# Kernel tuning notes

Measured on AMD Instinct MI355X. Metric: run time of the kernel, lower is better.

Reference implementation:

```python
import jax, jax.numpy as jnp
import numpy as np

NUM_HEADS = 4
LN_EPS = 1e-5


def rotate_half(x):
    x1 = x[..., ::2]
    x2 = x[..., 1::2]
    return jnp.stack((-x2, x1), axis=-1).reshape(x.shape)


def apply_rope(freqs, t):
    # freqs: [2, B, 1, S, hd] (cos, sin); t: [B, H, S, hd]
    return t * freqs[0] + rotate_half(t) * freqs[1]


def normalize_kpts(kpts):
    size = 1.0 + kpts.max(-2) - kpts.min(-2)          # [B, 2]
    shift = size / 2.0
    scale = size.max(-1) / 2.0                         # [B]
    return (kpts - shift[..., None, :]) / scale[..., None, None]


def posenc(kpts, Wr):
    proj = kpts @ Wr                                   # [B, S, hd//2]
    emb = jnp.stack([jnp.cos(proj), jnp.sin(proj)], 0)[:, :, None, :, :]  # [2,B,1,S,hd//2]
    return jnp.repeat(emb, 2, axis=-1)                 # [2, B, 1, S, hd]


def layer_norm(x, g, b):
    mu = x.mean(-1, keepdims=True)
    var = ((x - mu) ** 2).mean(-1, keepdims=True)
    return (x - mu) / jnp.sqrt(var + LN_EPS) * g + b


def ffn(x, W1, b1, g, bt, W2, b2):
    return jax.nn.gelu(layer_norm(x @ W1 + b1, g, bt), approximate=False) @ W2 + b2


def heads_split(t, H):  # [B,S,D] -> [B,H,S,hd]
    B, S, D = t.shape
    return t.reshape(B, S, H, D // H).transpose(0, 2, 1, 3)


def heads_merge(t):  # [B,H,S,hd] -> [B,S,D]
    B, H, S, hd = t.shape
    return t.transpose(0, 2, 1, 3).reshape(B, S, H * hd)


def self_block(x, enc, Wqkv, bqkv, Wo, bo, W1, b1, g, bt, W2, b2):
    B, S, D = x.shape
    H = NUM_HEADS
    hd = D // H
    qkv = (x @ Wqkv + bqkv).reshape(B, S, H, hd, 3).transpose(0, 2, 1, 3, 4)
    q, k, v = qkv[..., 0], qkv[..., 1], qkv[..., 2]
    q = apply_rope(enc, q)
    k = apply_rope(enc, k)
    sim = jnp.einsum('bhid,bhjd->bhij', q, k) * (hd ** -0.5)
    ctx = jnp.einsum('bhij,bhjd->bhid', jax.nn.softmax(sim, axis=-1), v)
    msg = heads_merge(ctx) @ Wo + bo
    return x + ffn(jnp.concatenate([x, msg], axis=-1), W1, b1, g, bt, W2, b2)


def cross_block(x0, x1, Wqk, bqk, Wv, bv, Wo, bo, W1, b1, g, bt, W2, b2):
    H = NUM_HEADS
    hd = x0.shape[-1] // H
    qk0 = heads_split(x0 @ Wqk + bqk, H)
    qk1 = heads_split(x1 @ Wqk + bqk, H)
    v0 = heads_split(x0 @ Wv + bv, H)
    v1 = heads_split(x1 @ Wv + bv, H)
    sc = hd ** -0.25  # scale**0.5 applied to each of qk0, qk1
    sim = jnp.einsum('bhid,bhjd->bhij', qk0 * sc, qk1 * sc)
    m0 = jnp.einsum('bhij,bhjd->bhid', jax.nn.softmax(sim, axis=-1), v1)
    m1 = jnp.einsum('bhij,bhid->bhjd', jax.nn.softmax(sim, axis=-2), v0)
    m0 = heads_merge(m0) @ Wo + bo
    m1 = heads_merge(m1) @ Wo + bo
    x0 = x0 + ffn(jnp.concatenate([x0, m0], axis=-1), W1, b1, g, bt, W2, b2)
    x1 = x1 + ffn(jnp.concatenate([x1, m1], axis=-1), W1, b1, g, bt, W2, b2)
    return x0, x1


def setup_inputs() -> dict:
    key = jax.random.key(0)
    ks = iter(jax.random.split(key, 64))
    B, M, N, D, L = 2, 1024, 1024, 256, 9
    hd = D // NUM_HEADS
    def nrm(shape, scale):
        return jax.random.normal(next(ks), shape, jnp.float32) * scale
    s = 1.0 / np.sqrt(D)
    s2 = 1.0 / np.sqrt(2 * D)
    return {
        'kpts0': jax.random.uniform(next(ks), (B, M, 2), jnp.float32) * 1024.0,
        'kpts1': jax.random.uniform(next(ks), (B, N, 2), jnp.float32) * 1024.0,
        'desc0': nrm((B, M, D), 1.0),
        'desc1': nrm((B, N, D), 1.0),
        'Wr': nrm((2, hd // 2), 1.0),
        'Win': nrm((D, D), s), 'b_in': jnp.zeros(D),
        'sWqkv': nrm((L, D, 3 * D), s), 'sbqkv': jnp.zeros((L, 3 * D)),
        'sWo': nrm((L, D, D), s), 'sbo': jnp.zeros((L, D)),
        'sW1': nrm((L, 2 * D, 2 * D), s2), 'sb1': jnp.zeros((L, 2 * D)),
        'sg': jnp.ones((L, 2 * D)), 'sbt': jnp.zeros((L, 2 * D)),
        'sW2': nrm((L, 2 * D, D), s2), 'sb2': jnp.zeros((L, D)),
        'cWqk': nrm((L, D, D), s), 'cbqk': jnp.zeros((L, D)),
        'cWv': nrm((L, D, D), s), 'cbv': jnp.zeros((L, D)),
        'cWo': nrm((L, D, D), s), 'cbo': jnp.zeros((L, D)),
        'cW1': nrm((L, 2 * D, 2 * D), s2), 'cb1': jnp.zeros((L, 2 * D)),
        'cg': jnp.ones((L, 2 * D)), 'cbt': jnp.zeros((L, 2 * D)),
        'cW2': nrm((L, 2 * D, D), s2), 'cb2': jnp.zeros((L, D)),
        'Wf': nrm((D, D), s), 'bf': jnp.zeros(D),
        'Wlv': nrm((D, 2), s), 'blv': jnp.zeros(2),
    }


def reference(kpts0, kpts1, desc0, desc1, Wr, Win, b_in,
              sWqkv, sbqkv, sWo, sbo, sW1, sb1, sg, sbt, sW2, sb2,
              cWqk, cbqk, cWv, cbv, cWo, cbo, cW1, cb1, cg, cbt, cW2, cb2,
              Wf, bf, Wlv, blv):
    enc0 = posenc(normalize_kpts(kpts0), Wr)
    enc1 = posenc(normalize_kpts(kpts1), Wr)
    x0 = desc0 @ Win + b_in
    x1 = desc1 @ Win + b_in
    for l in range(sWqkv.shape[0]):
        x0 = self_block(x0, enc0, sWqkv[l], sbqkv[l], sWo[l], sbo[l],
                        sW1[l], sb1[l], sg[l], sbt[l], sW2[l], sb2[l])
        x1 = self_block(x1, enc1, sWqkv[l], sbqkv[l], sWo[l], sbo[l],
                        sW1[l], sb1[l], sg[l], sbt[l], sW2[l], sb2[l])
        x0, x1 = cross_block(x0, x1, cWqk[l], cbqk[l], cWv[l], cbv[l], cWo[l], cbo[l],
                             cW1[l], cb1[l], cg[l], cbt[l], cW2[l], cb2[l])
    d = x0.shape[-1]
    md0 = (x0 @ Wf + bf) / d ** 0.25
    md1 = (x1 @ Wf + bf) / d ** 0.25
    sim = jnp.einsum('bmd,bnd->bmn', md0, md1)
    p_rp_01 = jax.nn.softmax(sim, axis=-1)
    p_rp_10 = jax.nn.softmax(sim, axis=-2)  # == softmax(sim^T, -1)^T
    logvar_01 = x0 @ Wlv + blv
    logvar_10 = x1 @ Wlv + blv
    return (p_rp_01, p_rp_10, logvar_01, logvar_10)
```

## Files before the change

### kernel.cpp

```cpp
#include <hip/hip_runtime.h>
#include <hip/hip_bf16.h>
#include <math.h>

using bf16 = __hip_bfloat16;
typedef __attribute__((ext_vector_type(8))) short short8;
typedef __attribute__((ext_vector_type(4))) float f32x4;

#define LOG2E 1.44269504f

__device__ __forceinline__ float bf2f(bf16 x){ return __bfloat162float(x); }
__device__ __forceinline__ bf16  f2bf(float x){ return __float2bfloat16(x); }
__device__ __forceinline__ float ldin(const void* p, size_t i, int f){
  return f ? ((const float*)p)[i] : bf2f(((const bf16*)p)[i]);
}
__device__ __forceinline__ void stout(void* out, size_t i, float v, int f){
  if (f) ((float*)out)[i] = v; else ((bf16*)out)[i] = f2bf(v);
}
__device__ __forceinline__ void split2(float v, bf16* hi, bf16* lo){
  bf16 h = f2bf(v); *hi = h; *lo = f2bf(v - bf2f(h));
}
#define MFMA(a, b, c) __builtin_amdgcn_mfma_f32_16x16x32_bf16(a, b, c, 0, 0, 0)

__global__ void sniff_kernel(const unsigned* __restrict__ sg, int* __restrict__ flag)
{
  if (threadIdx.x == 0 && blockIdx.x == 0) *flag = (sg[0] == 0x3F800000u) ? 1 : 0;
}

__global__ __launch_bounds__(256) void cvtf_kernel(const void* __restrict__ src, float* __restrict__ dst,
                                                   int n, const int* __restrict__ flag)
{
  int f = *flag;
  int i = blockIdx.x * 256 + threadIdx.x;
  if (i < n) dst[i] = ldin(src, i, f);
}

__global__ __launch_bounds__(256) void splitin_kernel(const void* __restrict__ src,
                                                      bf16* __restrict__ hi, bf16* __restrict__ lo,
                                                      int n, const int* __restrict__ flag)
{
  int f = *flag;
  int i = blockIdx.x * 256 + threadIdx.x;
  if (i < n) split2(ldin(src, i, f), &hi[i], &lo[i]);
}

template<bool ADDC>
__global__ __launch_bounds__(256) void gemm2_kernel(
    const bf16* __restrict__ Ahi, const bf16* __restrict__ Alo,
    const bf16* __restrict__ Bhi, const bf16* __restrict__ Blo,
    float* __restrict__ C, bf16* __restrict__ Chi, bf16* __restrict__ Clo,
    const float* __restrict__ bias,
    int K, int lda, int ldb, int ldc, int ldcp,
    long sAb, long sBb, long sCb, float scale)
{
  int z = blockIdx.z;
  Ahi += (size_t)z * sAb; Alo += (size_t)z * sAb;
  Bhi += (size_t)z * sBb; Blo += (size_t)z * sBb;
  size_t coff = (size_t)z * sCb;
  const int bm = blockIdx.y * 64, bn = blockIdx.x * 64;
  __shared__ bf16 AsH[64][72], AsL[64][72], BsH[64][72], BsL[64][72];
  const int tid  = threadIdx.x;
  const int lane = tid & 63, wid = tid >> 6;
  const int wr = wid >> 1, wc = wid & 1;
  const int srow = tid >> 2, sch = (tid & 3) * 8;
  const int lr = lane & 15, kg = (lane >> 4) * 8;
  f32x4 zero = {0.f, 0.f, 0.f, 0.f};
  f32x4 acc[2][2] = {{zero, zero}, {zero, zero}};
  for (int kt = 0; kt < K; kt += 64) {
    __syncthreads();
    size_t arow = (size_t)(bm + srow) * lda + kt + sch;
    size_t brow = (size_t)(bn + srow) * ldb + kt + sch;
    *(short8*)&AsH[srow][sch]      = *(const short8*)&Ahi[arow];
    *(short8*)&AsH[srow][sch + 32] = *(const short8*)&Ahi[arow + 32];
    *(short8*)&AsL[srow][sch]      = *(const short8*)&Alo[arow];
    *(short8*)&AsL[srow][sch + 32] = *(const short8*)&Alo[arow + 32];
    *(short8*)&BsH[srow][sch]      = *(const short8*)&Bhi[brow];
    *(short8*)&BsH[srow][sch + 32] = *(const short8*)&Bhi[brow + 32];
    *(short8*)&BsL[srow][sch]      = *(const short8*)&Blo[brow];
    *(short8*)&BsL[srow][sch + 32] = *(const short8*)&Blo[brow + 32];
    __syncthreads();
    #pragma unroll
    for (int kk = 0; kk < 2; kk++) {
      int kc = kk * 32 + kg;
      short8 ah0 = *(const short8*)&AsH[wr * 32 + lr][kc];
      short8 ah1 = *(const short8*)&AsH[wr * 32 + 16 + lr][kc];
      short8 al0 = *(const short8*)&AsL[wr * 32 + lr][kc];
      short8 al1 = *(const short8*)&AsL[wr * 32 + 16 + lr][kc];
      short8 bh0 = *(const short8*)&BsH[wc * 32 + lr][kc];
      short8 bh1 = *(const short8*)&BsH[wc * 32 + 16 + lr][kc];
      short8 bl0 = *(const short8*)&BsL[wc * 32 + lr][kc];
      short8 bl1 = *(const short8*)&BsL[wc * 32 + 16 + lr][kc];
      acc[0][0] = MFMA(ah0, bh0, acc[0][0]);
      acc[0][1] = MFMA(ah0, bh1, acc[0][1]);
      acc[1][0] = MFMA(ah1, bh0, acc[1][0]);
      acc[1][1] = MFMA(ah1, bh1, acc[1][1]);
      acc[0][0] = MFMA(ah0, bl0, acc[0][0]);
      acc[0][1] = MFMA(ah0, bl1, acc[0][1]);
      acc[1][0] = MFMA(ah1, bl0, acc[1][0]);
      acc[1][1] = MFMA(ah1, bl1, acc[1][1]);
      acc[0][0] = MFMA(al0, bh0, acc[0][0]);
      acc[0][1] = MFMA(al0, bh1, acc[0][1]);
      acc[1][0] = MFMA(al1, bh0, acc[1][0]);
      acc[1][1] = MFMA(al1, bh1, acc[1][1]);
    }
  }
  #pragma unroll
  for (int i = 0; i < 2; i++)
    #pragma unroll
    for (int j = 0; j < 2; j++) {
      int col = bn + wc * 32 + j * 16 + lr;
      float bv = bias ? bias[col] : 0.f;
      #pragma unroll
      for (int r = 0; r < 4; r++) {
        int row = bm + wr * 32 + i * 16 + (lane >> 4) * 4 + r;
        float v = (acc[i][j][r] + bv) * scale;
        if (C) {
          size_t idx = coff + (size_t)row * ldc + col;
          if (ADDC) v += C[idx];
          C[idx] = v;
        }
        if (Chi) {
          size_t idxp = (size_t)row * ldcp + col;
          split2(v, &Chi[idxp], &Clo[idxp]);
        }
      }
    }
}

template<bool ADDC>
static void gemm2(hipStream_t st, const bf16* Ahi, const bf16* Alo, const bf16* Bhi, const bf16* Blo,
                  float* C, bf16* Chi, bf16* Clo, const float* bias,
                  int M, int N, int K, int lda, int ldb, int ldc, int ldcp,
                  int Z, long sAb, long sBb, long sCb, float scale)
{
  dim3 g(N / 64, M / 64, Z);
  gemm2_kernel<ADDC><<<g, 256, 0, st>>>(Ahi, Alo, Bhi, Blo, C, Chi, Clo, bias,
                                        K, lda, ldb, ldc, ldcp, sAb, sBb, sCb, scale);
}

__global__ __launch_bounds__(256) void fattn_kernel(
    const bf16* __restrict__ Qh, const bf16* __restrict__ Ql,
    const bf16* __restrict__ Kh, const bf16* __restrict__ Kl,
    const bf16* __restrict__ Vh, const bf16* __restrict__ Vl,
    bf16* __restrict__ Oh, bf16* __restrict__ Ol,
    int ldq, int ldo, int cross, float scale)
{
  const int S = 1024;
  int z = blockIdx.y;
  size_t qoff, koff, voff, ooff;
  if (!cross) {
    qoff = (size_t)z * S * 64; koff = qoff;
    voff = (size_t)z * 64 * S;
    ooff = (size_t)(z >> 2) * S * 256 + (size_t)(z & 3) * 64;
  } else {
    int dir = z >> 3, b = (z >> 2) & 1, h = z & 3;
    size_t off0 = (size_t)b * S * 256 + (size_t)h * 64;
    size_t off1 = (size_t)(2048 + b * 1024) * 256 + (size_t)h * 64;
    if (dir == 0) { qoff = off0; koff = off1; voff = (size_t)(8 + b * 4 + h) * 64 * S; ooff = off0; }
    else          { qoff = off1; koff = off0; voff = (size_t)(b * 4 + h) * 64 * S;     ooff = off1; }
  }
  __shared__ bf16 KsH[64][72], KsL[64][72], VsH[64][72], VsL[64][72];
  __shared__ bf16 PsH[4][16][72], PsL[4][16][72];
  const int tid = threadIdx.x;
  const int lane = tid & 63, w = tid >> 6;
  const int lr = lane & 15, kg8 = (lane >> 4) * 8;
  const int q0 = blockIdx.x * 64;
  const float sl2 = scale * LOG2E;
  int qrow = q0 + (w << 4) + lr;
  short8 aQh[2], aQl[2];
  #pragma unroll
  for (int kk = 0; kk < 2; kk++) {
    size_t qi = qoff + (size_t)qrow * ldq + kk * 32 + kg8;
    aQh[kk] = *(const short8*)&Qh[qi];
    aQl[kk] = *(const short8*)&Ql[qi];
  }
  f32x4 zero = {0.f, 0.f, 0.f, 0.f};
  f32x4 accO[4] = {zero, zero, zero, zero};
  float m[4] = {-1e30f, -1e30f, -1e30f, -1e30f};
  float l[4] = {0.f, 0.f, 0.f, 0.f};
  const int srow = tid >> 2, sch = (tid & 3) * 8;
  for (int kt = 0; kt < 16; kt++) {
    __syncthreads();
    size_t ki = koff + (size_t)(kt * 64 + srow) * ldq + sch;
    size_t vi = voff + (size_t)srow * S + kt * 64 + sch;
    *(short8*)&KsH[srow][sch]      = *(const short8*)&Kh[ki];
    *(short8*)&KsH[srow][sch + 32] = *(const short8*)&Kh[ki + 32];
    *(short8*)&KsL[srow][sch]      = *(const short8*)&Kl[ki];
    *(short8*)&KsL[srow][sch + 32] = *(const short8*)&Kl[ki + 32];
    *(short8*)&VsH[srow][sch]      = *(const short8*)&Vh[vi];
    *(short8*)&VsH[srow][sch + 32] = *(const short8*)&Vh[vi + 32];
    *(short8*)&VsL[srow][sch]      = *(const short8*)&Vl[vi];
    *(short8*)&VsL[srow][sch + 32] = *(const short8*)&Vl[vi + 32];
    __syncthreads();
    f32x4 s[4] = {zero, zero, zero, zero};
    #pragma unroll
    for (int kk = 0; kk < 2; kk++)
      #pragma unroll
      for (int j = 0; j < 4; j++) {
        short8 bh = *(const short8*)&KsH[j * 16 + lr][kk * 32 + kg8];
        short8 bl = *(const short8*)&KsL[j * 16 + lr][kk * 32 + kg8];
        s[j] = MFMA(aQh[kk], bh, s[j]);
        s[j] = MFMA(aQh[kk], bl, s[j]);
        s[j] = MFMA(aQl[kk], bh, s[j]);
      }
    #pragma unroll
    for (int j = 0; j < 4; j++)
      #pragma unroll
      for (int r = 0; r < 4; r++) s[j][r] *= sl2;
    float fac[4], rs[4];
    #pragma unroll
    for (int r = 0; r < 4; r++) {
      float v = fmaxf(fmaxf(s[0][r], s[1][r]), fmaxf(s[2][r], s[3][r]));
      #pragma unroll
      for (int o = 8; o; o >>= 1) v = fmaxf(v, __shfl_xor(v, o));
      float nm = fmaxf(m[r], v);
      fac[r] = exp2f(m[r] - nm);
      m[r] = nm;
      rs[r] = 0.f;
    }
    #pragma unroll
    for (int j = 0; j < 4; j++)
      #pragma unroll
      for (int r = 0; r < 4; r++) {
        float p = exp2f(s[j][r] - m[r]);
        s[j][r] = p;
        rs[r] += p;
      }
    #pragma unroll
    for (int r = 0; r < 4; r++) {
      float v = rs[r];
      #pragma unroll
      for (int o = 8; o; o >>= 1) v += __shfl_xor(v, o);
      l[r] = l[r] * fac[r] + v;
      #pragma unroll
      for (int n = 0; n < 4; n++) accO[n][r] *= fac[r];
    }
    #pragma unroll
    for (int j = 0; j < 4; j++)
      #pragma unroll
      for (int r = 0; r < 4; r++)
        split2(s[j][r], &PsH[w][(lane >> 4) * 4 + r][j * 16 + lr],
                        &PsL[w][(lane >> 4) * 4 + r][j * 16 + lr]);
    __syncthreads();
    #pragma unroll
    for (int kk = 0; kk < 2; kk++) {
      short8 pah = *(const short8*)&PsH[w][lr][kk * 32 + kg8];
      short8 pal = *(const short8*)&PsL[w][lr][kk * 32 + kg8];
      #pragma unroll
      for (int n = 0; n < 4; n++) {
        short8 vh = *(const short8*)&VsH[n * 16 + lr][kk * 32 + kg8];
        short8 vl = *(const short8*)&VsL[n * 16 + lr][kk * 32 + kg8];
        accO[n] = MFMA(pah, vh, accO[n]);
        accO[n] = MFMA(pah, vl, accO[n]);
        accO[n] = MFMA(pal, vh, accO[n]);
      }
    }
  }
  #pragma unroll
  for (int n = 0; n < 4; n++)
    #pragma unroll
    for (int r = 0; r < 4; r++) {
      float v = accO[n][r] / l[r];
      int row = q0 + (w << 4) + (lane >> 4) * 4 + r;
      int col = n * 16 + lr;
      size_t idx = ooff + (size_t)row * ldo + col;
      split2(v, &Oh[idx], &Ol[idx]);
    }
}

__global__ __launch_bounds__(256) void transpose2_kernel(const void* __restrict__ src,
                                                         bf16* __restrict__ dhi, bf16* __restrict__ dlo,
                                                         int R, int C, const int* __restrict__ flag)
{
  __shared__ float tile[32][33];
  int f = *flag;
  size_t zoff = (size_t)blockIdx.z * R * C;
  int c0 = blockIdx.x * 32, r0 = blockIdx.y * 32;
  int x = threadIdx.x, y = threadIdx.y;
  for (int i = y; i < 32; i += 8)
    tile[i][x] = ldin(src, zoff + (size_t)(r0 + i) * C + (c0 + x), f);
  __syncthreads();
  for (int i = y; i < 32; i += 8) {
    size_t di = zoff + (size_t)(c0 + i) * R + (r0 + x);
    split2(tile[x][i], &dhi[di], &dlo[di]);
  }
}

__global__ __launch_bounds__(256) void minmax_kernel(const void* __restrict__ k0,
                                                     const void* __restrict__ k1,
                                                     float* __restrict__ mm, const int* __restrict__ flag)
{
  int f = *flag;
  int z = blockIdx.x;
  const void* kp = (z >= 2) ? k1 : k0;
  size_t base = (size_t)(z & 1) * 1024 * 2;
  int t = threadIdx.x;
  float mnx = 1e30f, mxx = -1e30f, mny = 1e30f, mxy = -1e30f;
  for (int s = t; s < 1024; s += 256) {
    float x = ldin(kp, base + s * 2, f), y = ldin(kp, base + s * 2 + 1, f);
    mnx = fminf(mnx, x); mxx = fmaxf(mxx, x);
    mny = fminf(mny, y); mxy = fmaxf(mxy, y);
  }
  for (int o = 32; o; o >>= 1) {
    mnx = fminf(mnx, __shfl_xor(mnx, o)); mxx = fmaxf(mxx, __shfl_xor(mxx, o));
    mny = fminf(mny, __shfl_xor(mny, o)); mxy = fmaxf(mxy, __shfl_xor(mxy, o));
  }
  __shared__ float r[4][4];
  if ((t & 63) == 0) { int w = t >> 6; r[w][0] = mnx; r[w][1] = mxx; r[w][2] = mny; r[w][3] = mxy; }
  __syncthreads();
  if (t == 0) {
    for (int w = 1; w < 4; w++) {
      r[0][0] = fminf(r[0][0], r[w][0]); r[0][1] = fmaxf(r[0][1], r[w][1]);
      r[0][2] = fminf(r[0][2], r[w][2]); r[0][3] = fmaxf(r[0][3], r[w][3]);
    }
    mm[z * 4 + 0] = r[0][0]; mm[z * 4 + 1] = r[0][1]; mm[z * 4 + 2] = r[0][2]; mm[z * 4 + 3] = r[0][3];
  }
}

__global__ __launch_bounds__(256) void posenc_kernel(const void* __restrict__ k0, const void* __restrict__ k1,
                                                     const float* __restrict__ mm, const void* __restrict__ Wr,
                                                     float* __restrict__ ecos, float* __restrict__ esin,
                                                     const int* __restrict__ flag)
{
  int f = *flag;
  int idx = blockIdx.x * 256 + threadIdx.x;
  int z = idx >> 10;
  const void* kp = (z >= 2) ? k1 : k0;
  size_t base = (size_t)(z & 1) * 1024 * 2 + (size_t)(idx & 1023) * 2;
  float sx = 1.f + mm[z * 4 + 1] - mm[z * 4 + 0];
  float sy = 1.f + mm[z * 4 + 3] - mm[z * 4 + 2];
  float scale = fmaxf(sx, sy) * 0.5f;
  float xn = (ldin(kp, base, f)     - sx * 0.5f) / scale;
  float yn = (ldin(kp, base + 1, f) - sy * 0.5f) / scale;
  for (int j = 0; j < 32; j++) {
    float p = xn * ldin(Wr, j, f) + yn * ldin(Wr, 32 + j, f);
    ecos[(size_t)idx * 32 + j] = cosf(p);
    esin[(size_t)idx * 32 + j] = sinf(p);
  }
}

__global__ __launch_bounds__(256) void rope_kernel(const float* __restrict__ qkv,
                                                   const float* __restrict__ ecos, const float* __restrict__ esin,
                                                   bf16* __restrict__ qh, bf16* __restrict__ ql,
                                                   bf16* __restrict__ kh, bf16* __restrict__ kl,
                                                   bf16* __restrict__ vh, bf16* __restrict__ vl)
{
  int idx = blockIdx.x * 256 + threadIdx.x;
  int row = idx >> 5, p = idx & 31;
  int zz = row >> 10, s = row & 1023;
  float c  = ecos[(size_t)row * 32 + p];
  float sn = esin[(size_t)row * 32 + p];
  const float* qp = qkv + (size_t)row * 768;
  #pragma unroll
  for (int h = 0; h < 4; h++) {
    int base = h * 192 + p * 6;
    float q0 = qp[base + 0], k0 = qp[base + 1], v0 = qp[base + 2];
    float q1 = qp[base + 3], k1 = qp[base + 4], v1 = qp[base + 5];
    int zh = zz * 4 + h;
    size_t qo = ((size_t)zh * 1024 + s) * 64 + 2 * p;
    split2(q0 * c - q1 * sn, &qh[qo],     &ql[qo]);
    split2(q1 * c + q0 * sn, &qh[qo + 1], &ql[qo + 1]);
    split2(k0 * c - k1 * sn, &kh[qo],     &kl[qo]);
    split2(k1 * c + k0 * sn, &kh[qo + 1], &kl[qo + 1]);
    size_t vo = ((size_t)zh * 64 + 2 * p) * 1024 + s;
    split2(v0, &vh[vo],        &vl[vo]);
    split2(v1, &vh[vo + 1024], &vl[vo + 1024]);
  }
}

__global__ __launch_bounds__(256) void vsplitT_kernel(const bf16* __restrict__ vhi, const bf16* __restrict__ vlo,
                                                      bf16* __restrict__ vThi, bf16* __restrict__ vTlo)
{
  __shared__ bf16 tile[32][33];
  int zz = blockIdx.z >> 1, plane = blockIdx.z & 1;
  const bf16* v  = plane ? vlo  : vhi;
  bf16*       vT = plane ? vTlo : vThi;
  int h = blockIdx.y >> 1, d0 = (blockIdx.y & 1) * 32;
  int s0 = blockIdx.x * 32;
  int x = threadIdx.x, y = threadIdx.y;
  const bf16* sp = v + ((size_t)zz * 1024 + s0) * 256 + h * 64 + d0;
  for (int i = y; i < 32; i += 8) tile[i][x] = sp[(size_t)i * 256 + x];
  __syncthreads();
  bf16* dp = vT + (((size_t)(zz * 4 + h)) * 64 + d0) * 1024 + s0;
  for (int i = y; i < 32; i += 8) dp[(size_t)i * 1024 + x] = tile[x][i];
}

__global__ __launch_bounds__(256) void row_softmax_kernel(const float* __restrict__ in,
                                                          void* __restrict__ outp, size_t eoff,
                                                          const int* __restrict__ flagp)
{
  int f = *flagp;
  size_t row = blockIdx.x;
  const float* ip = in + row * 1024;
  int t = threadIdx.x;
  float v[4]; float mx = -1e30f;
  #pragma unroll
  for (int i = 0; i < 4; i++) { v[i] = ip[t + i * 256] * LOG2E; mx = fmaxf(mx, v[i]); }
  #pragma unroll
  for (int o = 32; o; o >>= 1) mx = fmaxf(mx, __shfl_xor(mx, o));
  __shared__ float red[4];
  if ((t & 63) == 0) red[t >> 6] = mx;
  __syncthreads();
  mx = fmaxf(fmaxf(red[0], red[1]), fmaxf(red[2], red[3]));
  float sm = 0.f;
  #pragma unroll
  for (int i = 0; i < 4; i++) { v[i] = exp2f(v[i] - mx); sm += v[i]; }
  #pragma unroll
  for (int o = 32; o; o >>= 1) sm += __shfl_xor(sm, o);
  __shared__ float red2[4];
  if ((t & 63) == 0) red2[t >> 6] = sm;
  __syncthreads();
  sm = red2[0] + red2[1] + red2[2] + red2[3];
  float inv = 1.f / sm;
  size_t ob = eoff + row * 1024;
  #pragma unroll
  for (int i = 0; i < 4; i++) stout(outp, ob + t + i * 256, v[i] * inv, f);
}

__global__ __launch_bounds__(256) void col_softmax_kernel(const float* __restrict__ sim, void* __restrict__ out,
                                                          size_t eoff, const int* __restrict__ flagp)
{
  int f = *flagp;
  int b = blockIdx.y;
  int tid = threadIdx.x;
  int lane = tid & 63, w = tid >> 6;
  int lc = tid & 15;
  int g  = tid >> 4;
  int c = blockIdx.x * 16 + lc;
  const float* sp = sim + (size_t)b * 1048576 + c;
  float mx = -1e30f;
  for (int r = g; r < 1024; r += 16) mx = fmaxf(mx, sp[(size_t)r * 1024]);
  mx = fmaxf(mx, __shfl_xor(mx, 16));
  mx = fmaxf(mx, __shfl_xor(mx, 32));
  __shared__ float redm[4][16], reds[4][16];
  if ((lane >> 4) == 0) redm[w][lc] = mx;
  __syncthreads();
  mx = fmaxf(fmaxf(redm[0][lc], redm[1][lc]), fmaxf(redm[2][lc], redm[3][lc]));
  mx *= LOG2E;
  float sm = 0.f;
  for (int r = g; r < 1024; r += 16) sm += exp2f(sp[(size_t)r * 1024] * LOG2E - mx);
  sm += __shfl_xor(sm, 16);
  sm += __shfl_xor(sm, 32);
  if ((lane >> 4) == 0) reds[w][lc] = sm;
  __syncthreads();
  sm = reds[0][lc] + reds[1][lc] + reds[2][lc] + reds[3][lc];
  float inv = 1.f / sm;
  size_t ob = eoff + (size_t)b * 1048576 + c;
  for (int r = g; r < 1024; r += 16)
    stout(out, ob + (size_t)r * 1024, exp2f(sp[(size_t)r * 1024] * LOG2E - mx) * inv, f);
}

__global__ __launch_bounds__(256) void ln_gelu_kernel(const bf16* __restrict__ hh, const bf16* __restrict__ hl,
                                                      bf16* __restrict__ oh, bf16* __restrict__ ol,
                                                      const float* __restrict__ g, const float* __restrict__ bt)
{
  size_t row = blockIdx.x;
  const bf16 *hp = hh + row * 512, *lp = hl + row * 512;
  int t = threadIdx.x;
  float a = bf2f(hp[t]) + bf2f(lp[t]);
  float b = bf2f(hp[t + 256]) + bf2f(lp[t + 256]);
  float s = a + b, s2 = a * a + b * b;
  #pragma unroll
  for (int o = 32; o; o >>= 1) { s += __shfl_xor(s, o); s2 += __shfl_xor(s2, o); }
  __shared__ float r1[4], r2[4];
  if ((t & 63) == 0) { r1[t >> 6] = s; r2[t >> 6] = s2; }
  __syncthreads();
  s = r1[0] + r1[1] + r1[2] + r1[3];
  s2 = r2[0] + r2[1] + r2[2] + r2[3];
  float mu = s * (1.f / 512.f);
  float var = s2 * (1.f / 512.f) - mu * mu;
  float inv = rsqrtf(var + 1e-5f);
  float o1 = (a - mu) * inv * g[t] + bt[t];
  float o2 = (b - mu) * inv * g[t + 256] + bt[t + 256];
  o1 = 0.5f * o1 * (1.f + erff(o1 * 0.70710678118f));
  o2 = 0.5f * o2 * (1.f + erff(o2 * 0.70710678118f));
  split2(o1, &oh[row * 512 + t],       &ol[row * 512 + t]);
  split2(o2, &oh[row * 512 + t + 256], &ol[row * 512 + t + 256]);
}

__global__ __launch_bounds__(256) void logvar_kernel(const float* __restrict__ x, const void* __restrict__ Wlv,
                                                     const void* __restrict__ blv, void* __restrict__ out,
                                                     size_t eoff, const int* __restrict__ flagp)
{
  int f = *flagp;
  int idx = blockIdx.x * 256 + threadIdx.x;
  int r = idx >> 1, c = idx & 1;
  float acc = ldin(blv, c, f);
  const float* xp = x + (size_t)r * 256;
  for (int d = 0; d < 256; d++) acc += xp[d] * ldin(Wlv, d * 2 + c, f);
  int img = r >> 11, rs = r & 2047;
  stout(out, eoff + (size_t)img * 4096 + rs * 2 + c, acc, f);
}

extern "C" void kernel_launch(void* const* d_in, const int* in_sizes, int n_in,
                              void* d_out, int out_size, void* d_ws, size_t ws_size,
                              hipStream_t stream)
{
  (void)in_sizes; (void)n_in; (void)out_size; (void)ws_size;
  const int L = 9, S = 1024;
  const long SS = (long)S * S;
  char* w = (char*)d_ws; size_t off = 0;
  auto alloc = [&](size_t bytes) -> void* {
    void* p = w + off; off = (off + bytes + 1023) & ~(size_t)1023; return p;
  };
  struct Pair { bf16 *hi, *lo; };
  auto apair = [&](size_t elems) -> Pair {
    Pair p; p.hi = (bf16*)alloc(elems * 2); p.lo = (bf16*)alloc(elems * 2); return p;
  };
  int*   flag  = (int*)alloc(4);
  float* mm    = (float*)alloc(16 * 4);
  float* b_in  = (float*)alloc(256 * 4);
  float* sbqkv = (float*)alloc((size_t)L * 768 * 4);
  float* sbo   = (float*)alloc((size_t)L * 256 * 4);
  float* sb1   = (float*)alloc((size_t)L * 512 * 4);
  float* sg    = (float*)alloc((size_t)L * 512 * 4);
  float* sbt   = (float*)alloc((size_t)L * 512 * 4);
  float* sb2   = (float*)alloc((size_t)L * 256 * 4);
  float* cbqk  = (float*)alloc((size_t)L * 256 * 4);
  float* cbv   = (float*)alloc((size_t)L * 256 * 4);
  float* cbo   = (float*)alloc((size_t)L * 256 * 4);
  float* cb1   = (float*)alloc((size_t)L * 512 * 4);
  float* cg    = (float*)alloc((size_t)L * 512 * 4);
  float* cbt   = (float*)alloc((size_t)L * 512 * 4);
  float* cb2   = (float*)alloc((size_t)L * 256 * 4);
  float* bfv   = (float*)alloc(256 * 4);
  Pair WinT   = apair(65536);
  Pair WfT    = apair(65536);
  Pair sWqkvT = apair((size_t)L * 196608);
  Pair sWoT   = apair((size_t)L * 65536);
  Pair sW1T   = apair((size_t)L * 262144);
  Pair sW2T   = apair((size_t)L * 131072);
  Pair cWqkT  = apair((size_t)L * 65536);
  Pair cWvT   = apair((size_t)L * 65536);
  Pair cWoT   = apair((size_t)L * 65536);
  Pair cW1T   = apair((size_t)L * 262144);
  Pair cW2T   = apair((size_t)L * 131072);
  float* ecos  = (float*)alloc((size_t)4 * S * 32 * 4);
  float* esin  = (float*)alloc((size_t)4 * S * 32 * 4);
  float* xall  = (float*)alloc((size_t)4096 * 256 * 4);
  Pair qP      = apair((size_t)16 * S * 64);
  Pair kP      = apair((size_t)16 * S * 64);
  Pair vTP     = apair((size_t)16 * 64 * S);
  Pair catP    = apair((size_t)4096 * 512);
  Pair hmP     = apair((size_t)4096 * 512);
  Pair ctxP    = apair((size_t)4096 * 256);
  float* qkvb  = (float*)alloc((size_t)4096 * 768 * 4);
  float* simf  = (float*)alloc((size_t)2 * SS * 4);
  bf16* XH = catP.hi;
  bf16* XL = catP.lo;
  Pair qk2P  = {(bf16*)qkvb, (bf16*)qkvb + (size_t)4096 * 256};
  Pair v2P   = {(bf16*)qkvb + (size_t)2 * 4096 * 256, (bf16*)qkvb + (size_t)3 * 4096 * 256};
  Pair xinP  = {(bf16*)qkvb, (bf16*)qkvb + (size_t)4096 * 256};
  Pair mdP   = {(bf16*)qkvb, (bf16*)qkvb + (size_t)4096 * 256};

  sniff_kernel<<<1, 64, 0, stream>>>((const unsigned*)d_in[13], flag);

  auto cvtf = [&](const void* src, float* dst, int n) {
    cvtf_kernel<<<(n + 255) / 256, 256, 0, stream>>>(src, dst, n, flag);
  };
  cvtf(d_in[6],  b_in,  256);
  cvtf(d_in[8],  sbqkv, L * 768);
  cvtf(d_in[10], sbo,   L * 256);
  cvtf(d_in[12], sb1,   L * 512);
  cvtf(d_in[13], sg,    L * 512);
  cvtf(d_in[14], sbt,   L * 512);
  cvtf(d_in[16], sb2,   L * 256);
  cvtf(d_in[18], cbqk,  L * 256);
  cvtf(d_in[20], cbv,   L * 256);
  cvtf(d_in[22], cbo,   L * 256);
  cvtf(d_in[24], cb1,   L * 512);
  cvtf(d_in[25], cg,    L * 512);
  cvtf(d_in[26], cbt,   L * 512);
  cvtf(d_in[28], cb2,   L * 256);
  cvtf(d_in[30], bfv,   256);

  dim3 tb(32, 8);
  transpose2_kernel<<<dim3(8, 8, 1), tb, 0, stream>>>(d_in[5],  WinT.hi,   WinT.lo,   256, 256, flag);
  transpose2_kernel<<<dim3(8, 8, 1), tb, 0, stream>>>(d_in[29], WfT.hi,    WfT.lo,    256, 256, flag);
  transpose2_kernel<<<dim3(24, 8, L), tb, 0, stream>>>(d_in[7],  sWqkvT.hi, sWqkvT.lo, 256, 768, flag);
  transpose2_kernel<<<dim3(8, 8, L), tb, 0, stream>>>(d_in[9],  sWoT.hi,   sWoT.lo,   256, 256, flag);
  transpose2_kernel<<<dim3(16, 16, L), tb, 0, stream>>>(d_in[11], sW1T.hi,  sW1T.lo,  512, 512, flag);
  transpose2_kernel<<<dim3(8, 16, L), tb, 0, stream>>>(d_in[15], sW2T.hi,   sW2T.lo,  512, 256, flag);
  transpose2_kernel<<<dim3(8, 8, L), tb, 0, stream>>>(d_in[17], cWqkT.hi,  cWqkT.lo,  256, 256, flag);
  transpose2_kernel<<<dim3(8, 8, L), tb, 0, stream>>>(d_in[19], cWvT.hi,   cWvT.lo,   256, 256, flag);
  transpose2_kernel<<<dim3(8, 8, L), tb, 0, stream>>>(d_in[21], cWoT.hi,   cWoT.lo,   256, 256, flag);
  transpose2_kernel<<<dim3(16, 16, L), tb, 0, stream>>>(d_in[23], cW1T.hi,  cW1T.lo,  512, 512, flag);
  transpose2_kernel<<<dim3(8, 16, L), tb, 0, stream>>>(d_in[27], cW2T.hi,   cW2T.lo,  512, 256, flag);

  minmax_kernel<<<4, 256, 0, stream>>>(d_in[0], d_in[1], mm, flag);
  posenc_kernel<<<16, 256, 0, stream>>>(d_in[0], d_in[1], mm, d_in[4], ecos, esin, flag);

  splitin_kernel<<<2048, 256, 0, stream>>>(d_in[2], xinP.hi, xinP.lo, 2048 * 256, flag);
  splitin_kernel<<<2048, 256, 0, stream>>>(d_in[3], xinP.hi + (size_t)2048 * 256,
                                           xinP.lo + (size_t)2048 * 256, 2048 * 256, flag);
  gemm2<false>(stream, xinP.hi, xinP.lo, WinT.hi, WinT.lo, xall, XH, XL, b_in,
               4096, 256, 256, 256, 256, 256, 512, 1, 0, 0, 0, 1.f);

  for (int l = 0; l < L; l++) {
    gemm2<false>(stream, XH, XL, sWqkvT.hi + (size_t)l * 196608, sWqkvT.lo + (size_t)l * 196608,
                 qkvb, nullptr, nullptr, sbqkv + l * 768,
                 4096, 768, 256, 512, 256, 768, 0, 1, 0, 0, 0, 1.f);
    rope_kernel<<<512, 256, 0, stream>>>(qkvb, ecos, esin, qP.hi, qP.lo, kP.hi, kP.lo, vTP.hi, vTP.lo);
    fattn_kernel<<<dim3(16, 16), 256, 0, stream>>>(qP.hi, qP.lo, kP.hi, kP.lo, vTP.hi, vTP.lo,
                                                   ctxP.hi, ctxP.lo, 64, 256, 0, 0.125f);
    gemm2<false>(stream, ctxP.hi, ctxP.lo, sWoT.hi + (size_t)l * 65536, sWoT.lo + (size_t)l * 65536,
                 nullptr, catP.hi + 256, catP.lo + 256, sbo + l * 256,
                 4096, 256, 256, 256, 256, 0, 512, 1, 0, 0, 0, 1.f);
    gemm2<false>(stream, catP.hi, catP.lo, sW1T.hi + (size_t)l * 262144, sW1T.lo + (size_t)l * 262144,
                 nullptr, hmP.hi, hmP.lo, sb1 + l * 512,
                 4096, 512, 512, 512, 512, 0, 512, 1, 0, 0, 0, 1.f);
    ln_gelu_kernel<<<4096, 256, 0, stream>>>(hmP.hi, hmP.lo, hmP.hi, hmP.lo, sg + l * 512, sbt + l * 512);
    gemm2<true>(stream, hmP.hi, hmP.lo, sW2T.hi + (size_t)l * 131072, sW2T.lo + (size_t)l * 131072,
                xall, XH, XL, sb2 + l * 256,
                4096, 256, 512, 512, 512, 256, 512, 1, 0, 0, 0, 1.f);

    gemm2<false>(stream, XH, XL, cWqkT.hi + (size_t)l * 65536, cWqkT.lo + (size_t)l * 65536,
                 nullptr, qk2P.hi, qk2P.lo, cbqk + l * 256,
                 4096, 256, 256, 512, 256, 0, 256, 1, 0, 0, 0, 1.f);
    gemm2<false>(stream, XH, XL, cWvT.hi + (size_t)l * 65536, cWvT.lo + (size_t)l * 65536,
                 nullptr, v2P.hi, v2P.lo, cbv + l * 256,
                 4096, 256, 256, 512, 256, 0, 256, 1, 0, 0, 0, 1.f);
    vsplitT_kernel<<<dim3(32, 8, 8), tb, 0, stream>>>(v2P.hi, v2P.lo, vTP.hi, vTP.lo);
    fattn_kernel<<<dim3(16, 16), 256, 0, stream>>>(qk2P.hi, qk2P.lo, qk2P.hi, qk2P.lo, vTP.hi, vTP.lo,
                                                   ctxP.hi, ctxP.lo, 256, 256, 1, 0.125f);
    gemm2<false>(stream, ctxP.hi, ctxP.lo, cWoT.hi + (size_t)l * 65536, cWoT.lo + (size_t)l * 65536,
                 nullptr, catP.hi + 256, catP.lo + 256, cbo + l * 256,
                 4096, 256, 256, 256, 256, 0, 512, 1, 0, 0, 0, 1.f);
    gemm2<false>(stream, catP.hi, catP.lo, cW1T.hi + (size_t)l * 262144, cW1T.lo + (size_t)l * 262144,
                 nullptr, hmP.hi, hmP.lo, cb1 + l * 512,
                 4096, 512, 512, 512, 512, 0, 512, 1, 0, 0, 0, 1.f);
    ln_gelu_kernel<<<4096, 256, 0, stream>>>(hmP.hi, hmP.lo, hmP.hi, hmP.lo, cg + l * 512, cbt + l * 512);
    gemm2<true>(stream, hmP.hi, hmP.lo, cW2T.hi + (size_t)l * 131072, cW2T.lo + (size_t)l * 131072,
                xall, XH, XL, cb2 + l * 256,
                4096, 256, 512, 512, 512, 256, 512, 1, 0, 0, 0, 1.f);
  }

  gemm2<false>(stream, XH, XL, WfT.hi, WfT.lo, nullptr, mdP.hi, mdP.lo, bfv,
               4096, 256, 256, 512, 256, 0, 256, 1, 0, 0, 0, 0.25f);
  gemm2<false>(stream, mdP.hi, mdP.lo, mdP.hi + (size_t)2048 * 256, mdP.lo + (size_t)2048 * 256,
               simf, nullptr, nullptr, nullptr,
               1024, 1024, 256, 256, 256, 1024, 0, 2, (long)1024 * 256, (long)1024 * 256, SS, 1.f);
  row_softmax_kernel<<<2048, 256, 0, stream>>>(simf, d_out, 0, flag);
  col_softmax_kernel<<<dim3(64, 2), 256, 0, stream>>>(simf, d_out, 2097152, flag);
  logvar_kernel<<<32, 256, 0, stream>>>(xall, d_in[31], d_in[32], d_out, 4194304, flag);
}
```

Measured before the change: 2.202 ms.

## Split attention KV range across two blocks and fuse cross QK/V projections

The flash attention kernel now processes half of the key range per block (grid z=2) and writes unnormalized partial outputs plus row max and sum. A new combine kernel merges the two halves and emits hi/lo bf16 context, doubling the block count from 256 to 512 to fill more CUs. The cross-block QK and V projection weights are concatenated so a single GEMM with N=512 replaces two N=256 GEMMs, with strided V transpose. One __syncthreads between P write and P read is removed, which relies on per-wave private P tiles. The cost is extra fp32 partial traffic and an additional kernel launch per attention.

```diff
diff --git a/kernel.cpp b/kernel.cpp
--- a/kernel.cpp
+++ b/kernel.cpp
@@ -27,11 +27,12 @@
 }
 
 __global__ __launch_bounds__(256) void cvtf_kernel(const void* __restrict__ src, float* __restrict__ dst,
-                                                   int n, const int* __restrict__ flag)
+                                                   int n, int chunk, int ldd, int doff,
+                                                   const int* __restrict__ flag)
 {
   int f = *flag;
   int i = blockIdx.x * 256 + threadIdx.x;
-  if (i < n) dst[i] = ldin(src, i, f);
+  if (i < n) dst[(size_t)(i / chunk) * ldd + doff + (i % chunk)] = ldin(src, i, f);
 }
 
 __global__ __launch_bounds__(256) void splitin_kernel(const void* __restrict__ src,
@@ -141,22 +142,21 @@
     const bf16* __restrict__ Qh, const bf16* __restrict__ Ql,
     const bf16* __restrict__ Kh, const bf16* __restrict__ Kl,
     const bf16* __restrict__ Vh, const bf16* __restrict__ Vl,
-    bf16* __restrict__ Oh, bf16* __restrict__ Ol,
-    int ldq, int ldo, int cross, float scale)
+    float* __restrict__ pO, float* __restrict__ pm, float* __restrict__ pl,
+    int ldq, int cross, float scale)
 {
   const int S = 1024;
-  int z = blockIdx.y;
-  size_t qoff, koff, voff, ooff;
+  int z = blockIdx.y, half = blockIdx.z;
+  size_t qoff, koff, voff;
   if (!cross) {
     qoff = (size_t)z * S * 64; koff = qoff;
     voff = (size_t)z * 64 * S;
-    ooff = (size_t)(z >> 2) * S * 256 + (size_t)(z & 3) * 64;
   } else {
     int dir = z >> 3, b = (z >> 2) & 1, h = z & 3;
-    size_t off0 = (size_t)b * S * 256 + (size_t)h * 64;
-    size_t off1 = (size_t)(2048 + b * 1024) * 256 + (size_t)h * 64;
-    if (dir == 0) { qoff = off0; koff = off1; voff = (size_t)(8 + b * 4 + h) * 64 * S; ooff = off0; }
-    else          { qoff = off1; koff = off0; voff = (size_t)(b * 4 + h) * 64 * S;     ooff = off1; }
+    size_t off0 = (size_t)b * S * 512 + (size_t)h * 64;
+    size_t off1 = (size_t)(2048 + b * 1024) * 512 + (size_t)h * 64;
+    if (dir == 0) { qoff = off0; koff = off1; voff = (size_t)(8 + b * 4 + h) * 64 * S; }
+    else          { qoff = off1; koff = off0; voff = (size_t)(b * 4 + h) * 64 * S; }
   }
   __shared__ bf16 KsH[64][72], KsL[64][72], VsH[64][72], VsL[64][72];
   __shared__ bf16 PsH[4][16][72], PsL[4][16][72];
@@ -178,7 +178,7 @@
   float m[4] = {-1e30f, -1e30f, -1e30f, -1e30f};
   float l[4] = {0.f, 0.f, 0.f, 0.f};
   const int srow = tid >> 2, sch = (tid & 3) * 8;
-  for (int kt = 0; kt < 16; kt++) {
+  for (int kt = half * 8; kt < half * 8 + 8; kt++) {
     __syncthreads();
     size_t ki = koff + (size_t)(kt * 64 + srow) * ldq + sch;
     size_t vi = voff + (size_t)srow * S + kt * 64 + sch;
@@ -240,7 +240,6 @@
       for (int r = 0; r < 4; r++)
         split2(s[j][r], &PsH[w][(lane >> 4) * 4 + r][j * 16 + lr],
                         &PsL[w][(lane >> 4) * 4 + r][j * 16 + lr]);
-    __syncthreads();
     #pragma unroll
     for (int kk = 0; kk < 2; kk++) {
       short8 pah = *(const short8*)&PsH[w][lr][kk * 32 + kg8];
@@ -255,32 +254,66 @@
       }
     }
   }
+  int hz = half * 16 + z;
   #pragma unroll
   for (int n = 0; n < 4; n++)
     #pragma unroll
     for (int r = 0; r < 4; r++) {
-      float v = accO[n][r] / l[r];
       int row = q0 + (w << 4) + (lane >> 4) * 4 + r;
-      int col = n * 16 + lr;
-      size_t idx = ooff + (size_t)row * ldo + col;
-      split2(v, &Oh[idx], &Ol[idx]);
-    }
+      pO[((size_t)hz * 1024 + row) * 64 + n * 16 + lr] = accO[n][r];
+    }
+  if (lr == 0) {
+    #pragma unroll
+    for (int r = 0; r < 4; r++) {
+      int row = q0 + (w << 4) + (lane >> 4) * 4 + r;
+      pm[(size_t)hz * 1024 + row] = m[r];
+      pl[(size_t)hz * 1024 + row] = l[r];
+    }
+  }
+}
+
+__global__ __launch_bounds__(256) void fattn_combine_kernel(
+    const float* __restrict__ pO, const float* __restrict__ pm, const float* __restrict__ pl,
+    bf16* __restrict__ Oh, bf16* __restrict__ Ol, int cross)
+{
+  const int S = 1024;
+  int idx = blockIdx.x * 256 + threadIdx.x;
+  int col = idx & 63;
+  int row = (idx >> 6) & 1023;
+  int z = idx >> 16;
+  size_t r0 = (size_t)z * 1024 + row, r1 = r0 + 16 * 1024;
+  float m0 = pm[r0], m1 = pm[r1];
+  float M = fmaxf(m0, m1);
+  float e0 = exp2f(m0 - M), e1 = exp2f(m1 - M);
+  float den = pl[r0] * e0 + pl[r1] * e1;
+  float v = (pO[r0 * 64 + col] * e0 + pO[r1 * 64 + col] * e1) / den;
+  size_t ooff;
+  if (!cross) ooff = (size_t)(z >> 2) * S * 256 + (size_t)(z & 3) * 64;
+  else {
+    int dir = z >> 3, b = (z >> 2) & 1, h = z & 3;
+    ooff = dir == 0 ? (size_t)b * S * 256 + (size_t)h * 64
+                    : (size_t)(2048 + b * 1024) * 256 + (size_t)h * 64;
+  }
+  size_t oi = ooff + (size_t)row * 256 + col;
+  split2(v, &Oh[oi], &Ol[oi]);
 }
 
 __global__ __launch_bounds__(256) void transpose2_kernel(const void* __restrict__ src,
                                                          bf16* __restrict__ dhi, bf16* __restrict__ dlo,
-                                                         int R, int C, const int* __restrict__ flag)
+                                                         int R, int C, long sDstZ, long dOff,
+                                                         const int* __restrict__ flag)
 {
   __shared__ float tile[32][33];
   int f = *flag;
-  size_t zoff = (size_t)blockIdx.z * R * C;
+  size_t zsrc = (size_t)blockIdx.z * R * C;
+  size_t zdst = (size_t)blockIdx.z * sDstZ + dOff;
   int c0 = blockIdx.x * 32, r0 = blockIdx.y * 32;
   int x = threadIdx.x, y = threadIdx.y;
   for (int i = y; i < 32; i += 8)
-    tile[i][x] = ldin(src, zoff + (size_t)(r0 + i) * C + (c0 + x), f);
+    tile[i][x] = ldin(src, zsrc + (size_t)(r0 + i) * C + (c0 + x), f);
   __syncthreads();
   for (int i = y; i < 32; i += 8) {
-    size_t di = zoff + (size_t)(c0 + i) * R + (r0 + x);
+    size_t di = zdst + (size_t)(c0 + i) * R + (r0 + x);
     split2(tile[x][i], &dhi[di], &dlo[di]);
   }
 }
@@ -368,7 +401,7 @@
 }
 
 __global__ __launch_bounds__(256) void vsplitT_kernel(const bf16* __restrict__ vhi, const bf16* __restrict__ vlo,
-                                                      bf16* __restrict__ vThi, bf16* __restrict__ vTlo)
+                                                      bf16* __restrict__ vThi, bf16* __restrict__ vTlo, int ld)
 {
   __shared__ bf16 tile[32][33];
   int zz = blockIdx.z >> 1, plane = blockIdx.z & 1;
@@ -377,8 +410,8 @@
   int h = blockIdx.y >> 1, d0 = (blockIdx.y & 1) * 32;
   int s0 = blockIdx.x * 32;
   int x = threadIdx.x, y = threadIdx.y;
-  const bf16* sp = v + ((size_t)zz * 1024 + s0) * 256 + h * 64 + d0;
-  for (int i = y; i < 32; i += 8) tile[i][x] = sp[(size_t)i * 256 + x];
+  const bf16* sp = v + ((size_t)zz * 1024 + s0) * ld + h * 64 + d0;
+  for (int i = y; i < 32; i += 8) tile[i][x] = sp[(size_t)i * ld + x];
   __syncthreads();
   bf16* dp = vT + (((size_t)(zz * 4 + h)) * 64 + d0) * 1024 + s0;
   for (int i = y; i < 32; i += 8) dp[(size_t)i * 1024 + x] = tile[x][i];
@@ -515,8 +548,7 @@
   float* sg    = (float*)alloc((size_t)L * 512 * 4);
   float* sbt   = (float*)alloc((size_t)L * 512 * 4);
   float* sb2   = (float*)alloc((size_t)L * 256 * 4);
-  float* cbqk  = (float*)alloc((size_t)L * 256 * 4);
-  float* cbv   = (float*)alloc((size_t)L * 256 * 4);
+  float* cbqkv = (float*)alloc((size_t)L * 512 * 4);
   float* cbo   = (float*)alloc((size_t)L * 256 * 4);
   float* cb1   = (float*)alloc((size_t)L * 512 * 4);
   float* cg    = (float*)alloc((size_t)L * 512 * 4);
@@ -529,8 +561,7 @@
   Pair sWoT   = apair((size_t)L * 65536);
   Pair sW1T   = apair((size_t)L * 262144);
   Pair sW2T   = apair((size_t)L * 131072);
-  Pair cWqkT  = apair((size_t)L * 65536);
-  Pair cWvT   = apair((size_t)L * 65536);
+  Pair cWqkvT = apair((size_t)L * 131072);
   Pair cWoT   = apair((size_t)L * 65536);
   Pair cW1T   = apair((size_t)L * 262144);
   Pair cW2T   = apair((size_t)L * 131072);
@@ -544,18 +575,20 @@
   Pair hmP     = apair((size_t)4096 * 512);
   Pair ctxP    = apair((size_t)4096 * 256);
   float* qkvb  = (float*)alloc((size_t)4096 * 768 * 4);
-  float* simf  = (float*)alloc((size_t)2 * SS * 4);
+  float* pO    = (float*)alloc((size_t)2 * 16 * 1024 * 64 * 4);
+  float* pm    = (float*)alloc((size_t)32 * 1024 * 4);
+  float* pl    = (float*)alloc((size_t)32 * 1024 * 4);
+  float* simf  = pO;
   bf16* XH = catP.hi;
   bf16* XL = catP.lo;
-  Pair qk2P  = {(bf16*)qkvb, (bf16*)qkvb + (size_t)4096 * 256};
-  Pair v2P   = {(bf16*)qkvb + (size_t)2 * 4096 * 256, (bf16*)qkvb + (size_t)3 * 4096 * 256};
+  Pair qkv2P = {(bf16*)qkvb, (bf16*)qkvb + (size_t)4096 * 512};
   Pair xinP  = {(bf16*)qkvb, (bf16*)qkvb + (size_t)4096 * 256};
   Pair mdP   = {(bf16*)qkvb, (bf16*)qkvb + (size_t)4096 * 256};
 
   sniff_kernel<<<1, 64, 0, stream>>>((const unsigned*)d_in[13], flag);
 
   auto cvtf = [&](const void* src, float* dst, int n) {
-    cvtf_kernel<<<(n + 255) / 256, 256, 0, stream>>>(src, dst, n, flag);
+    cvtf_kernel<<<(n + 255) / 256, 256, 0, stream>>>(src, dst, n, n, n, 0, flag);
   };
   cvtf(d_in[6],  b_in,  256);
   cvtf(d_in[8],  sbqkv, L * 768);
@@ -564,8 +597,8 @@
   cvtf(d_in[13], sg,    L * 512);
   cvtf(d_in[14], sbt,   L * 512);
   cvtf(d_in[16], sb2,   L * 256);
-  cvtf(d_in[18], cbqk,  L * 256);
-  cvtf(d_in[20], cbv,   L * 256);
+  cvtf_kernel<<<(L * 256 + 255) / 256, 256, 0, stream>>>(d_in[18], cbqkv, L * 256, 256, 512, 0, flag);
+  cvtf_kernel<<<(L * 256 + 255) / 256, 256, 0, stream>>>(d_in[20], cbqkv, L * 256, 256, 512, 256, flag);
   cvtf(d_in[22], cbo,   L * 256);
   cvtf(d_in[24], cb1,   L * 512);
   cvtf(d_in[25], cg,    L * 512);
@@ -574,17 +607,17 @@
   cvtf(d_in[30], bfv,   256);
 
   dim3 tb(32, 8);
-  transpose2_kernel<<<dim3(8, 8, 1), tb, 0, stream>>>(d_in[5],  WinT.hi,   WinT.lo,   256, 256, flag);
-  transpose2_kernel<<<dim3(8, 8, 1), tb, 0, stream>>>(d_in[29], WfT.hi,    WfT.lo,    256, 256, flag);
-  transpose2_kernel<<<dim3(24, 8, L), tb, 0, stream>>>(d_in[7],  sWqkvT.hi, sWqkvT.lo, 256, 768, flag);
-  transpose2_kernel<<<dim3(8, 8, L), tb, 0, stream>>>(d_in[9],  sWoT.hi,   sWoT.lo,   256, 256, flag);
-  transpose2_kernel<<<dim3(16, 16, L), tb, 0, stream>>>(d_in[11], sW1T.hi,  sW1T.lo,  512, 512, flag);
-  transpose2_kernel<<<dim3(8, 16, L), tb, 0, stream>>>(d_in[15], sW2T.hi,   sW2T.lo,  512, 256, flag);
-  transpose2_kernel<<<dim3(8, 8, L), tb, 0, stream>>>(d_in[17], cWqkT.hi,  cWqkT.lo,  256, 256, flag);
-  transpose2_kernel<<<dim3(8, 8, L), tb, 0, stream>>>(d_in[19], cWvT.hi,   cWvT.lo,   256, 256, flag);
-  transpose2_kernel<<<dim3(8, 8, L), tb, 0, stream>>>(d_in[21], cWoT.hi,   cWoT.lo,   256, 256, flag);
-  transpose2_kernel<<<dim3(16, 16, L), tb, 0, stream>>>(d_in[23], cW1T.hi,  cW1T.lo,  512, 512, flag);
-  transpose2_kernel<<<dim3(8, 16, L), tb, 0, stream>>>(d_in[27], cW2T.hi,   cW2T.lo,  512, 256, flag);
+  transpose2_kernel<<<dim3(8, 8, 1), tb, 0, stream>>>(d_in[5],  WinT.hi,   WinT.lo,   256, 256, 65536, 0, flag);
+  transpose2_kernel<<<dim3(8, 8, 1), tb, 0, stream>>>(d_in[29], WfT.hi,    WfT.lo,    256, 256, 65536, 0, flag);
+  transpose2_kernel<<<dim3(24, 8, L), tb, 0, stream>>>(d_in[7],  sWqkvT.hi, sWqkvT.lo, 256, 768, 196608, 0, flag);
+  transpose2_kernel<<<dim3(8, 8, L), tb, 0, stream>>>(d_in[9],  sWoT.hi,   sWoT.lo,   256, 256, 65536, 0, flag);
+  transpose2_kernel<<<dim3(16, 16, L), tb, 0, stream>>>(d_in[11], sW1T.hi,  sW1T.lo,  512, 512, 262144, 0, flag);
+  transpose2_kernel<<<dim3(8, 16, L), tb, 0, stream>>>(d_in[15], sW2T.hi,   sW2T.lo,  512, 256, 131072, 0, flag);
+  transpose2_kernel<<<dim3(8, 8, L), tb, 0, stream>>>(d_in[17], cWqkvT.hi, cWqkvT.lo, 256, 256, 131072, 0, flag);
+  transpose2_kernel<<<dim3(8, 8, L), tb, 0, stream>>>(d_in[19], cWqkvT.hi, cWqkvT.lo, 256, 256, 131072, 65536, flag);
+  transpose2_kernel<<<dim3(8, 8, L), tb, 0, stream>>>(d_in[21], cWoT.hi,   cWoT.lo,   256, 256, 65536, 0, flag);
+  transpose2_kernel<<<dim3(16, 16, L), tb, 0, stream>>>(d_in[23], cW1T.hi,  cW1T.lo,  512, 512, 262144, 0, flag);
+  transpose2_kernel<<<dim3(8, 16, L), tb, 0, stream>>>(d_in[27], cW2T.hi,   cW2T.lo,  512, 256, 131072, 0, flag);
 
   minmax_kernel<<<4, 256, 0, stream>>>(d_in[0], d_in[1], mm, flag);
   posenc_kernel<<<16, 256, 0, stream>>>(d_in[0], d_in[1], mm, d_in[4], ecos, esin, flag);
@@ -600,8 +633,9 @@
                  qkvb, nullptr, nullptr, sbqkv + l * 768,
                  4096, 768, 256, 512, 256, 768, 0, 1, 0, 0, 0, 1.f);
     rope_kernel<<<512, 256, 0, stream>>>(qkvb, ecos, esin, qP.hi, qP.lo, kP.hi, kP.lo, vTP.hi, vTP.lo);
-    fattn_kernel<<<dim3(16, 16), 256, 0, stream>>>(qP.hi, qP.lo, kP.hi, kP.lo, vTP.hi, vTP.lo,
-                                                   ctxP.hi, ctxP.lo, 64, 256, 0, 0.125f);
+    fattn_kernel<<<dim3(16, 16, 2), 256, 0, stream>>>(qP.hi, qP.lo, kP.hi, kP.lo, vTP.hi, vTP.lo,
+                                                      pO, pm, pl, 64, 0, 0.125f);
+    fattn_combine_kernel<<<4096, 256, 0, stream>>>(pO, pm, pl, ctxP.hi, ctxP.lo, 0);
     gemm2<false>(stream, ctxP.hi, ctxP.lo, sWoT.hi + (size_t)l * 65536, sWoT.lo + (size_t)l * 65536,
                  nullptr, catP.hi + 256, catP.lo + 256, sbo + l * 256,
                  4096, 256, 256, 256, 256, 0, 512, 1, 0, 0, 0, 1.f);
@@ -613,15 +647,13 @@
                 xall, XH, XL, sb2 + l * 256,
                 4096, 256, 512, 512, 512, 256, 512, 1, 0, 0, 0, 1.f);
 
-    gemm2<false>(stream, XH, XL, cWqkT.hi + (size_t)l * 65536, cWqkT.lo + (size_t)l * 65536,
-                 nullptr, qk2P.hi, qk2P.lo, cbqk + l * 256,
-                 4096, 256, 256, 512, 256, 0, 256, 1, 0, 0, 0, 1.f);
-    gemm2<false>(stream, XH, XL, cWvT.hi + (size_t)l * 65536, cWvT.lo + (size_t)l * 65536,
-                 nullptr, v2P.hi, v2P.lo, cbv + l * 256,
-                 4096, 256, 256, 512, 256, 0, 256, 1, 0, 0, 0, 1.f);
-    vsplitT_kernel<<<dim3(32, 8, 8), tb, 0, stream>>>(v2P.hi, v2P.lo, vTP.hi, vTP.lo);
-    fattn_kernel<<<dim3(16, 16), 256, 0, stream>>>(qk2P.hi, qk2P.lo, qk2P.hi, qk2P.lo, vTP.hi, vTP.lo,
-                                                   ctxP.hi, ctxP.lo, 256, 256, 1, 0.125f);
+    gemm2<false>(stream, XH, XL, cWqkvT.hi + (size_t)l * 131072, cWqkvT.lo + (size_t)l * 131072,
+                 nullptr, qkv2P.hi, qkv2P.lo, cbqkv + l * 512,
+                 4096, 512, 256, 512, 256, 0, 512, 1, 0, 0, 0, 1.f);
+    vsplitT_kernel<<<dim3(32, 8, 8), tb, 0, stream>>>(qkv2P.hi + 256, qkv2P.lo + 256, vTP.hi, vTP.lo, 512);
+    fattn_kernel<<<dim3(16, 16, 2), 256, 0, stream>>>(qkv2P.hi, qkv2P.lo, qkv2P.hi, qkv2P.lo, vTP.hi, vTP.lo,
+                                                      pO, pm, pl, 512, 1, 0.125f);
+    fattn_combine_kernel<<<4096, 256, 0, stream>>>(pO, pm, pl, ctxP.hi, ctxP.lo, 1);
     gemm2<false>(stream, ctxP.hi, ctxP.lo, cWoT.hi + (size_t)l * 65536, cWoT.lo + (size_t)l * 65536,
                  nullptr, catP.hi + 256, catP.lo + 256, cbo + l * 256,
                  4096, 256, 256, 256, 256, 0, 512, 1, 0, 0, 0, 1.f);
```

Result: faster. 2.002 ms (-9.1%).
